# Kernel optimization log

Hardware: AMD Instinct MI355X
Metric: run time of the kernel (lower is better)

## Reference

```python
import jax, jax.numpy as jnp
import numpy as np

NEG_INF = float(np.finfo(np.float32).min)
CHUNK = 8
EPS = 1e-6
NOISE_STD = 1.0
SHARP = 1.0


def exclusive_cumsum(x):
    # [a,b,c] -> [0,a,a+b]
    return jnp.cumsum(jnp.pad(x[:, :-1], ((0, 0), (1, 0))), axis=1)


def moving_sum(x, back, forward):
    # x: [B, K]; out[i] = sum x[i-back : i+forward+1], via cumsum difference
    w = back + forward + 1
    xp = jnp.pad(x, ((0, 0), (back, forward)))
    cs = jnp.pad(jnp.cumsum(xp, axis=1), ((0, 0), (1, 0)))
    return cs[:, w:] - cs[:, :-w]


def setup_inputs() -> dict:
    key = jax.random.key(0)
    ks = jax.random.split(key, 12)
    B, K, D, A = 64, 2000, 512, 512
    s = 0.02
    inp = {
        'key': jax.random.normal(ks[0], (B, K, D), jnp.float32),
        'value': jax.random.normal(ks[1], (B, K, D), jnp.float32),
        'query': jax.random.normal(ks[2], (B, 1, D), jnp.float32),
        'mask': jnp.ones((B, 1, K), jnp.int32),
        'aw_prev': jnp.zeros((B, K), jnp.float32).at[:, 0].set(1.0),
        'noise': jax.random.normal(ks[3], (B, K), jnp.float32),
        'Wk_mono': jax.random.normal(ks[4], (D, A), jnp.float32) * s,
        'bk_mono': jnp.zeros((A,), jnp.float32),
        'Wq_mono': jax.random.normal(ks[5], (D, A), jnp.float32) * s,
        'bq_mono': jnp.zeros((A,), jnp.float32),
        'r': jnp.full((1,), -4.0, jnp.float32),
        'Wk_chunk': jax.random.normal(ks[6], (D, A), jnp.float32) * s,
        'bk_chunk': jnp.zeros((A,), jnp.float32),
        'Wq_chunk': jax.random.normal(ks[7], (D, A), jnp.float32) * s,
        'bq_chunk': jnp.zeros((A,), jnp.float32),
    }
    return inp


def reference(key, value, query, mask, aw_prev, noise,
              Wk_mono, bk_mono, Wq_mono, bq_mono, r,
              Wk_chunk, bk_chunk, Wq_chunk, bq_chunk):
    B, K, _ = key.shape
    adim = Wk_mono.shape[1]
    scale = jnp.sqrt(jnp.asarray(adim, jnp.float32))
    m = mask.reshape(B, K) != 0  # qlen == 1

    # ---- monotonic energy (scaled_dot) ----
    k_m = key @ Wk_mono + bk_mono              # [B,K,A]
    q_m = query @ Wq_mono + bq_mono            # [B,1,A]
    e_mono = jnp.einsum('bqa,bka->bk', q_m, k_m) / scale + r[0]
    e_mono = jnp.where(m, e_mono, NEG_INF)

    # ---- parallel-mode monotonic alignment ----
    p = jax.nn.sigmoid(e_mono + noise * NOISE_STD)             # p_choose_i
    cumprod_1mp = jnp.exp(exclusive_cumsum(jnp.log(jnp.clip(1.0 - p, EPS, 1.0))))
    alpha = p * cumprod_1mp * jnp.cumsum(
        aw_prev / jnp.clip(cumprod_1mp, EPS, 1.0), axis=1)     # [B,K]

    # ---- chunkwise attention ----
    k_c = key @ Wk_chunk + bk_chunk
    q_c = query @ Wq_chunk + bq_chunk
    e_c = jnp.einsum('bqa,bka->bk', q_c, k_c) / scale
    e_c = jnp.where(m, e_c, NEG_INF)
    e_c = e_c - jnp.max(e_c, axis=1, keepdims=True)
    sm_exp = jnp.clip(jnp.exp(e_c), 1e-5, None)
    denom = moving_sum(sm_exp, CHUNK - 1, 0)
    beta = sm_exp * moving_sum(alpha * SHARP / denom, 0, CHUNK - 1)  # [B,K]

    # ---- context vector ----
    cv = jnp.einsum('bk,bkd->bd', beta, value)[:, None, :]     # [B,1,D]
    return cv, alpha
```

## Files before the change

kernel.cpp:

```cpp
#include <hip/hip_runtime.h>
#include <hip/hip_bf16.h>

#define B_N    64
#define K_LEN  2000
#define D_DIM  512
#define NEG_INF (-3.402823466e38f)
#define EPS_C  1e-6f
#define INV_SCALE (1.0f/22.62741699796952f)

__global__ __launch_bounds__(256) void proj_kernel(
    const float* __restrict__ query,
    const float* __restrict__ Wq_m, const float* __restrict__ bq_m,
    const float* __restrict__ Wq_c, const float* __restrict__ bq_c,
    const float* __restrict__ Wk_m, const float* __restrict__ bk_m,
    const float* __restrict__ Wk_c, const float* __restrict__ bk_c,
    const float* __restrict__ r,
    float* __restrict__ v_all, float* __restrict__ c_all)
{
    const int b = blockIdx.x, br = blockIdx.y, t = threadIdx.x;
    const float* Wq = br ? Wq_c : Wq_m;
    const float* bq = br ? bq_c : bq_m;
    const float* Wk = br ? Wk_c : Wk_m;
    const float* bk = br ? bk_c : bk_m;
    __shared__ float qs[D_DIM];
    __shared__ float qv[D_DIM];
    __shared__ float red[256];
    for (int i = t; i < D_DIM; i += 256) qs[i] = query[(size_t)b*D_DIM + i];
    __syncthreads();
    for (int a = t; a < D_DIM; a += 256) {
        float a0 = 0.f, a1 = 0.f, a2 = 0.f, a3 = 0.f;
        #pragma unroll 4
        for (int d = 0; d < D_DIM; d += 4) {
            a0 = fmaf(qs[d+0], Wq[(size_t)(d+0)*D_DIM + a], a0);
            a1 = fmaf(qs[d+1], Wq[(size_t)(d+1)*D_DIM + a], a1);
            a2 = fmaf(qs[d+2], Wq[(size_t)(d+2)*D_DIM + a], a2);
            a3 = fmaf(qs[d+3], Wq[(size_t)(d+3)*D_DIM + a], a3);
        }
        qv[a] = (a0 + a1) + (a2 + a3) + bq[a];
    }
    __syncthreads();
    for (int d = t; d < D_DIM; d += 256) {
        const float4* row = (const float4*)(Wk + (size_t)d*D_DIM);
        const float4* q4 = (const float4*)qv;
        float acc = 0.f;
        #pragma unroll 4
        for (int a4 = 0; a4 < D_DIM/4; ++a4) {
            float4 w = row[a4], q = q4[a4];
            acc = fmaf(w.x, q.x, acc); acc = fmaf(w.y, q.y, acc);
            acc = fmaf(w.z, q.z, acc); acc = fmaf(w.w, q.w, acc);
        }
        v_all[((size_t)b*2 + br)*D_DIM + d] = acc * INV_SCALE;
    }
    float part = 0.f;
    for (int a = t; a < D_DIM; a += 256) part = fmaf(qv[a], bk[a], part);
    red[t] = part; __syncthreads();
    for (int s = 128; s; s >>= 1) { if (t < s) red[t] += red[t + s]; __syncthreads(); }
    if (t == 0) c_all[b*2 + br] = red[0] * INV_SCALE + (br ? 0.f : r[0]);
}

__global__ __launch_bounds__(256) void energy_kernel(
    const float* __restrict__ key, const int* __restrict__ mask,
    const float* __restrict__ v_all, const float* __restrict__ c_all,
    float* __restrict__ e_mono, float* __restrict__ e_c)
{
    const int b = blockIdx.x;
    const int kb0 = blockIdx.y * 125;
    const int kend = kb0 + 125;
    const int lane = threadIdx.x & 63;
    const int wave = threadIdx.x >> 6;
    const float4* vm4 = (const float4*)(v_all + ((size_t)b*2 + 0)*D_DIM);
    const float4* vc4 = (const float4*)(v_all + ((size_t)b*2 + 1)*D_DIM);
    const float4 vmA = vm4[lane*2], vmB = vm4[lane*2 + 1];
    const float4 vcA = vc4[lane*2], vcB = vc4[lane*2 + 1];
    const float cm = c_all[b*2 + 0], cc = c_all[b*2 + 1];

    for (int k = kb0 + wave; k < kend; k += 8) {
        const int k2 = k + 4;
        const bool has2 = (k2 < kend);
        const float4* kr0 = (const float4*)(key + ((size_t)b*K_LEN + k)*D_DIM);
        const float4* kr1 = (const float4*)(key + ((size_t)b*K_LEN + (has2 ? k2 : k))*D_DIM);
        float4 a0 = kr0[lane*2], b0 = kr0[lane*2 + 1];
        float4 a1 = kr1[lane*2], b1 = kr1[lane*2 + 1];
        float dm0 = 0.f, dc0 = 0.f, dm1 = 0.f, dc1 = 0.f;
        dm0 = fmaf(a0.x, vmA.x, dm0); dm0 = fmaf(a0.y, vmA.y, dm0);
        dm0 = fmaf(a0.z, vmA.z, dm0); dm0 = fmaf(a0.w, vmA.w, dm0);
        dm0 = fmaf(b0.x, vmB.x, dm0); dm0 = fmaf(b0.y, vmB.y, dm0);
        dm0 = fmaf(b0.z, vmB.z, dm0); dm0 = fmaf(b0.w, vmB.w, dm0);
        dc0 = fmaf(a0.x, vcA.x, dc0); dc0 = fmaf(a0.y, vcA.y, dc0);
        dc0 = fmaf(a0.z, vcA.z, dc0); dc0 = fmaf(a0.w, vcA.w, dc0);
        dc0 = fmaf(b0.x, vcB.x, dc0); dc0 = fmaf(b0.y, vcB.y, dc0);
        dc0 = fmaf(b0.z, vcB.z, dc0); dc0 = fmaf(b0.w, vcB.w, dc0);
        dm1 = fmaf(a1.x, vmA.x, dm1); dm1 = fmaf(a1.y, vmA.y, dm1);
        dm1 = fmaf(a1.z, vmA.z, dm1); dm1 = fmaf(a1.w, vmA.w, dm1);
        dm1 = fmaf(b1.x, vmB.x, dm1); dm1 = fmaf(b1.y, vmB.y, dm1);
        dm1 = fmaf(b1.z, vmB.z, dm1); dm1 = fmaf(b1.w, vmB.w, dm1);
        dc1 = fmaf(a1.x, vcA.x, dc1); dc1 = fmaf(a1.y, vcA.y, dc1);
        dc1 = fmaf(a1.z, vcA.z, dc1); dc1 = fmaf(a1.w, vcA.w, dc1);
        dc1 = fmaf(b1.x, vcB.x, dc1); dc1 = fmaf(b1.y, vcB.y, dc1);
        dc1 = fmaf(b1.z, vcB.z, dc1); dc1 = fmaf(b1.w, vcB.w, dc1);
        #pragma unroll
        for (int off = 32; off; off >>= 1) {
            dm0 += __shfl_xor(dm0, off); dc0 += __shfl_xor(dc0, off);
            dm1 += __shfl_xor(dm1, off); dc1 += __shfl_xor(dc1, off);
        }
        if (lane == 0) {
            size_t gk = (size_t)b*K_LEN + k;
            bool mk = mask[gk] != 0;
            e_mono[gk] = mk ? dm0 + cm : NEG_INF;
            e_c[gk]    = mk ? dc0 + cc : NEG_INF;
            if (has2) {
                size_t gk2 = (size_t)b*K_LEN + k2;
                bool mk2 = mask[gk2] != 0;
                e_mono[gk2] = mk2 ? dm1 + cm : NEG_INF;
                e_c[gk2]    = mk2 ? dc1 + cc : NEG_INF;
            }
        }
    }
}

__global__ __launch_bounds__(256) void scan_kernel(
    const float* __restrict__ e_mono_g, const float* __restrict__ e_c_g,
    const float* __restrict__ noise, const float* __restrict__ aw_prev,
    float* __restrict__ alpha_out, float* __restrict__ beta_out)
{
    const int b = blockIdx.x, t = threadIdx.x;
    const int lane = t & 63, wv = t >> 6;
    __shared__ float sal[2048];
    __shared__ float sse[2048];
    __shared__ float su[2048];
    __shared__ float wsA[4], wsB[4], wsM[4];

    const float* em = e_mono_g + (size_t)b*K_LEN;
    const float* ec = e_c_g   + (size_t)b*K_LEN;
    const float* nz = noise   + (size_t)b*K_LEN;
    const float* aw = aw_prev + (size_t)b*K_LEN;

    const int base = t*8;
    float p[8], lg[8];
    #pragma unroll
    for (int j = 0; j < 8; ++j) {
        const int k = base + j;
        float pv = 0.f, lv = 0.f, ecv = NEG_INF;
        if (k < K_LEN) {
            float e = em[k] + nz[k];
            pv = 1.f / (1.f + __expf(-e) * 1.0f);
            pv = 1.f / (1.f + expf(-e));
            float om = fminf(fmaxf(1.f - pv, EPS_C), 1.f);
            lv = logf(om);
            ecv = ec[k];
        }
        p[j] = pv; lg[j] = lv; sse[k] = ecv;
    }

    float ex[8]; float run = 0.f;
    #pragma unroll
    for (int j = 0; j < 8; ++j) { ex[j] = run; run += lg[j]; }
    float incl = run;
    #pragma unroll
    for (int off = 1; off < 64; off <<= 1) {
        float v = __shfl_up(incl, off, 64);
        if (lane >= off) incl += v;
    }
    if (lane == 63) wsA[wv] = incl;
    __syncthreads();
    float wpre = 0.f;
    #pragma unroll
    for (int w = 0; w < 4; ++w) if (w < wv) wpre += wsA[w];
    const float pre = wpre + incl - run;

    float cp[8], t2i[8]; float run2 = 0.f;
    #pragma unroll
    for (int j = 0; j < 8; ++j) {
        const int k = base + j;
        float c = expf(pre + ex[j]);
        cp[j] = c;
        float t2 = 0.f;
        if (k < K_LEN) t2 = aw[k] / fminf(fmaxf(c, EPS_C), 1.f);
        run2 += t2; t2i[j] = run2;
    }
    float incl2 = run2;
    #pragma unroll
    for (int off = 1; off < 64; off <<= 1) {
        float v = __shfl_up(incl2, off, 64);
        if (lane >= off) incl2 += v;
    }
    if (lane == 63) wsB[wv] = incl2;
    __syncthreads();
    float wpre2 = 0.f;
    #pragma unroll
    for (int w = 0; w < 4; ++w) if (w < wv) wpre2 += wsB[w];
    const float pre2 = wpre2 + incl2 - run2;
    #pragma unroll
    for (int j = 0; j < 8; ++j) {
        const int k = base + j;
        float al = p[j] * cp[j] * (pre2 + t2i[j]);
        sal[k] = al;
        if (k < K_LEN) alpha_out[(size_t)b*K_LEN + k] = al;
    }
    __syncthreads();

    float mx = NEG_INF;
    for (int k = t; k < 2048; k += 256) mx = fmaxf(mx, sse[k]);
    #pragma unroll
    for (int off = 32; off; off >>= 1) mx = fmaxf(mx, __shfl_xor(mx, off));
    if (lane == 0) wsM[wv] = mx;
    __syncthreads();
    mx = fmaxf(fmaxf(wsM[0], wsM[1]), fmaxf(wsM[2], wsM[3]));

    for (int k = t; k < 2048; k += 256) {
        float se = 0.f;
        if (k < K_LEN) se = fmaxf(expf(sse[k] - mx), 1e-5f);
        sse[k] = se;
    }
    __syncthreads();
    for (int k = t; k < 2048; k += 256) {
        float u = 0.f;
        if (k < K_LEN) {
            float den = 0.f;
            int j0 = (k > 7) ? (k - 7) : 0;
            for (int j = j0; j <= k; ++j) den += sse[j];
            u = sal[k] / den;
        }
        su[k] = u;
    }
    __syncthreads();
    for (int k = t; k < K_LEN; k += 256) {
        float s2 = 0.f;
        #pragma unroll
        for (int j = 0; j < 8; ++j) s2 += su[k + j];
        beta_out[(size_t)b*K_LEN + k] = sse[k] * s2;
    }
}

__global__ __launch_bounds__(256) void cv_part_kernel(
    const float* __restrict__ value, const float* __restrict__ beta,
    float* __restrict__ partial)
{
    const int b = blockIdx.x, s = blockIdx.y, t = threadIdx.x;
    const int f4 = t & 127, half = t >> 7;
    const int k0 = s * 100;
    __shared__ float bs[100];
    __shared__ float4 comb[128];
    if (t < 100) bs[t] = beta[(size_t)b*K_LEN + k0 + t];
    __syncthreads();
    float4 acc = {0.f, 0.f, 0.f, 0.f};
    for (int k = k0 + half; k < k0 + 100; k += 2) {
        float4 vv = ((const float4*)(value + ((size_t)b*K_LEN + k)*D_DIM))[f4];
        float bb = bs[k - k0];
        acc.x = fmaf(bb, vv.x, acc.x); acc.y = fmaf(bb, vv.y, acc.y);
        acc.z = fmaf(bb, vv.z, acc.z); acc.w = fmaf(bb, vv.w, acc.w);
    }
    if (half) comb[f4] = acc;
    __syncthreads();
    if (!half) {
        float4 o = comb[f4];
        acc.x += o.x; acc.y += o.y; acc.z += o.z; acc.w += o.w;
        ((float4*)(partial + ((size_t)b*20 + s)*D_DIM))[f4] = acc;
    }
}

__global__ __launch_bounds__(256) void cv_reduce_kernel(
    const float* __restrict__ partial, float* __restrict__ cv)
{
    const int idx = blockIdx.x*256 + threadIdx.x;
    const int b = idx >> 9, d = idx & 511;
    float acc = 0.f;
    #pragma unroll
    for (int s = 0; s < 20; ++s) acc += partial[((size_t)b*20 + s)*D_DIM + d];
    cv[idx] = acc;
}

extern "C" void kernel_launch(void* const* d_in, const int* in_sizes, int n_in,
                              void* d_out, int out_size, void* d_ws, size_t ws_size,
                              hipStream_t stream) {
    const float* key     = (const float*)d_in[0];
    const float* value   = (const float*)d_in[1];
    const float* query   = (const float*)d_in[2];
    const int*   mask    = (const int*)d_in[3];
    const float* aw_prev = (const float*)d_in[4];
    const float* noise   = (const float*)d_in[5];
    const float* Wk_m    = (const float*)d_in[6];
    const float* bk_m    = (const float*)d_in[7];
    const float* Wq_m    = (const float*)d_in[8];
    const float* bq_m    = (const float*)d_in[9];
    const float* r       = (const float*)d_in[10];
    const float* Wk_c    = (const float*)d_in[11];
    const float* bk_c    = (const float*)d_in[12];
    const float* Wq_c    = (const float*)d_in[13];
    const float* bq_c    = (const float*)d_in[14];

    float* out   = (float*)d_out;
    float* cv    = out;
    float* alpha = out + (size_t)B_N*D_DIM;

    float* ws      = (float*)d_ws;
    float* e_mono  = ws;
    float* e_c     = ws + 128000;
    float* beta    = ws + 256000;
    float* v_all   = ws + 384000;
    float* c_all   = ws + 449536;
    float* partial = ws + 449664;

    proj_kernel<<<dim3(B_N, 2), 256, 0, stream>>>(query, Wq_m, bq_m, Wq_c, bq_c,
                                                  Wk_m, bk_m, Wk_c, bk_c, r,
                                                  v_all, c_all);
    energy_kernel<<<dim3(B_N, 16), 256, 0, stream>>>(key, mask, v_all, c_all, e_mono, e_c);
    scan_kernel<<<B_N, 256, 0, stream>>>(e_mono, e_c, noise, aw_prev, alpha, beta);
    cv_part_kernel<<<dim3(B_N, 20), 256, 0, stream>>>(value, beta, partial);
    cv_reduce_kernel<<<32768/256, 256, 0, stream>>>(partial, cv);
}
```

Before: 614.3 us.

## Restructure energy dot-product mapping, vectorize scan loads, atomic-reduce context vector

The energy kernel now splits each 64-lane wave into four 16-lane groups, one key row per group. Each lane loads 8 contiguous float4s and keeps its slice of both query projections in registers, which shortens the shuffle reduction. The grid grows to 20 k-blocks of 100 rows. The scan kernel reads and writes with float4 accesses instead of scalar ones. The separate cv reduce kernel is removed: cv is zeroed in proj_kernel and partial sums are atomically added, saving a launch and the partial buffer at the cost of atomic contention and non-deterministic summation order.

```diff
diff --git a/kernel.cpp b/kernel.cpp
--- a/kernel.cpp
+++ b/kernel.cpp
@@ -15,9 +15,12 @@
     const float* __restrict__ Wk_m, const float* __restrict__ bk_m,
     const float* __restrict__ Wk_c, const float* __restrict__ bk_c,
     const float* __restrict__ r,
-    float* __restrict__ v_all, float* __restrict__ c_all)
+    float* __restrict__ v_all, float* __restrict__ c_all,
+    float* __restrict__ cv)
 {
     const int b = blockIdx.x, br = blockIdx.y, t = threadIdx.x;
+    cv[(size_t)b*D_DIM + br*256 + t] = 0.f;
+
     const float* Wq = br ? Wq_c : Wq_m;
     const float* bq = br ? bq_c : bq_m;
     const float* Wk = br ? Wk_c : Wk_m;
@@ -64,56 +67,45 @@
     float* __restrict__ e_mono, float* __restrict__ e_c)
 {
     const int b = blockIdx.x;
-    const int kb0 = blockIdx.y * 125;
-    const int kend = kb0 + 125;
+    const int kb0 = blockIdx.y * 100;
     const int lane = threadIdx.x & 63;
     const int wave = threadIdx.x >> 6;
-    const float4* vm4 = (const float4*)(v_all + ((size_t)b*2 + 0)*D_DIM);
-    const float4* vc4 = (const float4*)(v_all + ((size_t)b*2 + 1)*D_DIM);
-    const float4 vmA = vm4[lane*2], vmB = vm4[lane*2 + 1];
-    const float4 vcA = vc4[lane*2], vcB = vc4[lane*2 + 1];
+    const int sub  = lane & 15;
+    const int rsub = lane >> 4;
+
+    const float4* vmb = (const float4*)(v_all + ((size_t)b*2 + 0)*D_DIM) + sub*8;
+    const float4* vcb = (const float4*)(v_all + ((size_t)b*2 + 1)*D_DIM) + sub*8;
+    float4 vm[8], vc[8];
+    #pragma unroll
+    for (int i = 0; i < 8; ++i) vm[i] = vmb[i];
+    #pragma unroll
+    for (int i = 0; i < 8; ++i) vc[i] = vcb[i];
     const float cm = c_all[b*2 + 0], cc = c_all[b*2 + 1];
 
-    for (int k = kb0 + wave; k < kend; k += 8) {
-        const int k2 = k + 4;
-        const bool has2 = (k2 < kend);
-        const float4* kr0 = (const float4*)(key + ((size_t)b*K_LEN + k)*D_DIM);
-        const float4* kr1 = (const float4*)(key + ((size_t)b*K_LEN + (has2 ? k2 : k))*D_DIM);
-        float4 a0 = kr0[lane*2], b0 = kr0[lane*2 + 1];
-        float4 a1 = kr1[lane*2], b1 = kr1[lane*2 + 1];
-        float dm0 = 0.f, dc0 = 0.f, dm1 = 0.f, dc1 = 0.f;
-        dm0 = fmaf(a0.x, vmA.x, dm0); dm0 = fmaf(a0.y, vmA.y, dm0);
-        dm0 = fmaf(a0.z, vmA.z, dm0); dm0 = fmaf(a0.w, vmA.w, dm0);
-        dm0 = fmaf(b0.x, vmB.x, dm0); dm0 = fmaf(b0.y, vmB.y, dm0);
-        dm0 = fmaf(b0.z, vmB.z, dm0); dm0 = fmaf(b0.w, vmB.w, dm0);
-        dc0 = fmaf(a0.x, vcA.x, dc0); dc0 = fmaf(a0.y, vcA.y, dc0);
-        dc0 = fmaf(a0.z, vcA.z, dc0); dc0 = fmaf(a0.w, vcA.w, dc0);
-        dc0 = fmaf(b0.x, vcB.x, dc0); dc0 = fmaf(b0.y, vcB.y, dc0);
-        dc0 = fmaf(b0.z, vcB.z, dc0); dc0 = fmaf(b0.w, vcB.w, dc0);
-        dm1 = fmaf(a1.x, vmA.x, dm1); dm1 = fmaf(a1.y, vmA.y, dm1);
-        dm1 = fmaf(a1.z, vmA.z, dm1); dm1 = fmaf(a1.w, vmA.w, dm1);
-        dm1 = fmaf(b1.x, vmB.x, dm1); dm1 = fmaf(b1.y, vmB.y, dm1);
-        dm1 = fmaf(b1.z, vmB.z, dm1); dm1 = fmaf(b1.w, vmB.w, dm1);
-        dc1 = fmaf(a1.x, vcA.x, dc1); dc1 = fmaf(a1.y, vcA.y, dc1);
-        dc1 = fmaf(a1.z, vcA.z, dc1); dc1 = fmaf(a1.w, vcA.w, dc1);
-        dc1 = fmaf(b1.x, vcB.x, dc1); dc1 = fmaf(b1.y, vcB.y, dc1);
-        dc1 = fmaf(b1.z, vcB.z, dc1); dc1 = fmaf(b1.w, vcB.w, dc1);
-        #pragma unroll
-        for (int off = 32; off; off >>= 1) {
-            dm0 += __shfl_xor(dm0, off); dc0 += __shfl_xor(dc0, off);
-            dm1 += __shfl_xor(dm1, off); dc1 += __shfl_xor(dc1, off);
-        }
-        if (lane == 0) {
-            size_t gk = (size_t)b*K_LEN + k;
-            bool mk = mask[gk] != 0;
-            e_mono[gk] = mk ? dm0 + cm : NEG_INF;
-            e_c[gk]    = mk ? dc0 + cc : NEG_INF;
-            if (has2) {
-                size_t gk2 = (size_t)b*K_LEN + k2;
-                bool mk2 = mask[gk2] != 0;
-                e_mono[gk2] = mk2 ? dm1 + cm : NEG_INF;
-                e_c[gk2]    = mk2 ? dc1 + cc : NEG_INF;
-            }
+    for (int kg = kb0 + wave*4; kg < kb0 + 100; kg += 16) {
+        const int k = kg + rsub;
+        const float4* kr = (const float4*)(key + ((size_t)b*K_LEN + k)*D_DIM) + sub*8;
+        float4 x[8];
+        #pragma unroll
+        for (int i = 0; i < 8; ++i) x[i] = kr[i];
+        float dm = 0.f, dc = 0.f;
+        #pragma unroll
+        for (int i = 0; i < 8; ++i) {
+            dm = fmaf(x[i].x, vm[i].x, dm); dm = fmaf(x[i].y, vm[i].y, dm);
+            dm = fmaf(x[i].z, vm[i].z, dm); dm = fmaf(x[i].w, vm[i].w, dm);
+            dc = fmaf(x[i].x, vc[i].x, dc); dc = fmaf(x[i].y, vc[i].y, dc);
+            dc = fmaf(x[i].z, vc[i].z, dc); dc = fmaf(x[i].w, vc[i].w, dc);
+        }
+        #pragma unroll
+        for (int off = 8; off; off >>= 1) {
+            dm += __shfl_xor(dm, off);
+            dc += __shfl_xor(dc, off);
+        }
+        if (sub == 0) {
+            const size_t gk = (size_t)b*K_LEN + k;
+            const bool mk = mask[gk] != 0;
+            e_mono[gk] = mk ? dm + cm : NEG_INF;
+            e_c[gk]    = mk ? dc + cc : NEG_INF;
         }
     }
 }
@@ -136,20 +128,38 @@
     const float* aw = aw_prev + (size_t)b*K_LEN;
 
     const int base = t*8;
+    const bool inb = base < K_LEN;
+    float emv[8], nzv[8], ecv[8], awv[8];
+    if (inb) {
+        float4 a0 = ((const float4*)(em + base))[0], a1 = ((const float4*)(em + base))[1];
+        emv[0]=a0.x; emv[1]=a0.y; emv[2]=a0.z; emv[3]=a0.w;
+        emv[4]=a1.x; emv[5]=a1.y; emv[6]=a1.z; emv[7]=a1.w;
+        float4 n0 = ((const float4*)(nz + base))[0], n1 = ((const float4*)(nz + base))[1];
+        nzv[0]=n0.x; nzv[1]=n0.y; nzv[2]=n0.z; nzv[3]=n0.w;
+        nzv[4]=n1.x; nzv[5]=n1.y; nzv[6]=n1.z; nzv[7]=n1.w;
+        float4 c0 = ((const float4*)(ec + base))[0], c1 = ((const float4*)(ec + base))[1];
+        ecv[0]=c0.x; ecv[1]=c0.y; ecv[2]=c0.z; ecv[3]=c0.w;
+        ecv[4]=c1.x; ecv[5]=c1.y; ecv[6]=c1.z; ecv[7]=c1.w;
+        float4 w0 = ((const float4*)(aw + base))[0], w1 = ((const float4*)(aw + base))[1];
+        awv[0]=w0.x; awv[1]=w0.y; awv[2]=w0.z; awv[3]=w0.w;
+        awv[4]=w1.x; awv[5]=w1.y; awv[6]=w1.z; awv[7]=w1.w;
+    } else {
+        #pragma unroll
+        for (int j = 0; j < 8; ++j) { emv[j]=0.f; nzv[j]=0.f; ecv[j]=NEG_INF; awv[j]=0.f; }
+    }
+
     float p[8], lg[8];
     #pragma unroll
     for (int j = 0; j < 8; ++j) {
-        const int k = base + j;
-        float pv = 0.f, lv = 0.f, ecv = NEG_INF;
-        if (k < K_LEN) {
-            float e = em[k] + nz[k];
-            pv = 1.f / (1.f + __expf(-e) * 1.0f);
+        float pv = 0.f, lv = 0.f;
+        if (inb) {
+            float e = emv[j] + nzv[j];
             pv = 1.f / (1.f + expf(-e));
             float om = fminf(fmaxf(1.f - pv, EPS_C), 1.f);
             lv = logf(om);
-            ecv = ec[k];
-        }
-        p[j] = pv; lg[j] = lv; sse[k] = ecv;
+        }
+        p[j] = pv; lg[j] = lv;
+        sse[base + j] = inb ? ecv[j] : NEG_INF;
     }
 
     float ex[8]; float run = 0.f;
@@ -168,14 +178,12 @@
     for (int w = 0; w < 4; ++w) if (w < wv) wpre += wsA[w];
     const float pre = wpre + incl - run;
 
-    float cp[8], t2i[8]; float run2 = 0.f;
+    float cp_[8], t2i[8]; float run2 = 0.f;
     #pragma unroll
     for (int j = 0; j < 8; ++j) {
-        const int k = base + j;
         float c = expf(pre + ex[j]);
-        cp[j] = c;
-        float t2 = 0.f;
-        if (k < K_LEN) t2 = aw[k] / fminf(fmaxf(c, EPS_C), 1.f);
+        cp_[j] = c;
+        float t2 = inb ? awv[j] / fminf(fmaxf(c, EPS_C), 1.f) : 0.f;
         run2 += t2; t2i[j] = run2;
     }
     float incl2 = run2;
@@ -190,12 +198,17 @@
     #pragma unroll
     for (int w = 0; w < 4; ++w) if (w < wv) wpre2 += wsB[w];
     const float pre2 = wpre2 + incl2 - run2;
+
+    float al[8];
     #pragma unroll
     for (int j = 0; j < 8; ++j) {
-        const int k = base + j;
-        float al = p[j] * cp[j] * (pre2 + t2i[j]);
-        sal[k] = al;
-        if (k < K_LEN) alpha_out[(size_t)b*K_LEN + k] = al;
+        al[j] = p[j] * cp_[j] * (pre2 + t2i[j]);
+        sal[base + j] = al[j];
+    }
+    if (inb) {
+        float* ao = alpha_out + (size_t)b*K_LEN + base;
+        ((float4*)ao)[0] = make_float4(al[0], al[1], al[2], al[3]);
+        ((float4*)ao)[1] = make_float4(al[4], al[5], al[6], al[7]);
     }
     __syncthreads();
 
@@ -232,9 +245,9 @@
     }
 }
 
-__global__ __launch_bounds__(256) void cv_part_kernel(
+__global__ __launch_bounds__(256) void cv_kernel(
     const float* __restrict__ value, const float* __restrict__ beta,
-    float* __restrict__ partial)
+    float* __restrict__ cv)
 {
     const int b = blockIdx.x, s = blockIdx.y, t = threadIdx.x;
     const int f4 = t & 127, half = t >> 7;
@@ -254,20 +267,12 @@
     __syncthreads();
     if (!half) {
         float4 o = comb[f4];
-        acc.x += o.x; acc.y += o.y; acc.z += o.z; acc.w += o.w;
-        ((float4*)(partial + ((size_t)b*20 + s)*D_DIM))[f4] = acc;
-    }
-}
-
-__global__ __launch_bounds__(256) void cv_reduce_kernel(
-    const float* __restrict__ partial, float* __restrict__ cv)
-{
-    const int idx = blockIdx.x*256 + threadIdx.x;
-    const int b = idx >> 9, d = idx & 511;
-    float acc = 0.f;
-    #pragma unroll
-    for (int s = 0; s < 20; ++s) acc += partial[((size_t)b*20 + s)*D_DIM + d];
-    cv[idx] = acc;
+        float* dst = cv + (size_t)b*D_DIM + f4*4;
+        atomicAdd(dst + 0, acc.x + o.x);
+        atomicAdd(dst + 1, acc.y + o.y);
+        atomicAdd(dst + 2, acc.z + o.z);
+        atomicAdd(dst + 3, acc.w + o.w);
+    }
 }
 
 extern "C" void kernel_launch(void* const* d_in, const int* in_sizes, int n_in,
@@ -299,13 +304,11 @@
     float* beta    = ws + 256000;
     float* v_all   = ws + 384000;
     float* c_all   = ws + 449536;
-    float* partial = ws + 449664;
 
     proj_kernel<<<dim3(B_N, 2), 256, 0, stream>>>(query, Wq_m, bq_m, Wq_c, bq_c,
                                                   Wk_m, bk_m, Wk_c, bk_c, r,
-                                                  v_all, c_all);
-    energy_kernel<<<dim3(B_N, 16), 256, 0, stream>>>(key, mask, v_all, c_all, e_mono, e_c);
+                                                  v_all, c_all, cv);
+    energy_kernel<<<dim3(B_N, 20), 256, 0, stream>>>(key, mask, v_all, c_all, e_mono, e_c);
     scan_kernel<<<B_N, 256, 0, stream>>>(e_mono, e_c, noise, aw_prev, alpha, beta);
-    cv_part_kernel<<<dim3(B_N, 20), 256, 0, stream>>>(value, beta, partial);
-    cv_reduce_kernel<<<32768/256, 256, 0, stream>>>(partial, cv);
-}
+    cv_kernel<<<dim3(B_N, 20), 256, 0, stream>>>(value, beta, cv);
+}
```

Measured after the change: 619.3 us. No clear change (+0.8%).
